# Kernel optimization log

Measured on AMD Instinct MI355X. Metric: run time of the kernel, lower is better.

The kernel has to match this reference:

```python
import jax, jax.numpy as jnp
import numpy as np


def setup_inputs() -> dict:
    key = jax.random.key(0)
    k1, k2 = jax.random.split(key)
    B, H, W, C = 32, 32, 32, 256
    N_EMBED = 1024
    z = jax.random.normal(k1, (B, H, W, C), dtype=jnp.float32)
    emb_weights = jax.random.normal(k2, (N_EMBED, C), dtype=jnp.float32)
    return {"z": z, "emb_weights": emb_weights}


def reference(z, emb_weights):
    # z: (B,H,W,C) -> flatten to (N, C)
    B = z.shape[0]
    C = z.shape[-1]
    z_flat = z.reshape(-1, C)  # (N, C)
    # Squared euclidean distance via ||z||^2 + ||e||^2 - 2 z.e^T
    distance = (
        jnp.sum(z_flat ** 2, axis=1, keepdims=True)          # (N, 1)
        + jnp.sum(emb_weights ** 2, axis=1)                   # (n_embed,)
        - 2.0 * jnp.dot(z_flat, emb_weights.T)                # (N, n_embed)
    )
    min_encoding_indices = jnp.argmin(distance, axis=1)       # (N,)
    z_q = emb_weights[min_encoding_indices].reshape(z.shape)  # (B,H,W,C)
    min_encoding_indices = min_encoding_indices.reshape(B, -1)
    return z_q, min_encoding_indices
```

## Files before the change

kernel.cpp:

```cpp
#include <hip/hip_runtime.h>

#define C_DIM 256
#define NCODE 1024
#define MARGIN1 0.35f
#define MARGIN2 0.02f

typedef __bf16 bf16x8 __attribute__((ext_vector_type(8)));
typedef float f32x4 __attribute__((ext_vector_type(4)));

#define WS_ENORM  0
#define WS_META   4096
#define WS_RLIST  8192
#define WS_RLIST2 139264
#define WS_BP     270336
#define WS_PB     1318912
#define WS_PBI    1843200
#define WS_PB2    2105344
#define WS_PBI2   3153920

#define BP_LO_OFF 262144

#define GLOAD_LDS16(g, s)                                                            \
  __builtin_amdgcn_global_load_lds(                                                  \
      (const __attribute__((address_space(1))) unsigned int*)(g),                    \
      (__attribute__((address_space(3))) unsigned int*)(s), 16, 0, 0)

__device__ __forceinline__ unsigned short bf16rne(float x) {
    unsigned u = __float_as_uint(x);
    return (unsigned short)((u + 0x7FFFu + ((u >> 16) & 1u)) >> 16);
}
__device__ __forceinline__ void bf16split(float x, unsigned short& h, unsigned short& l) {
    unsigned u  = __float_as_uint(x);
    unsigned rh = (u + 0x7FFFu + ((u >> 16) & 1u)) & 0xFFFF0000u;
    float    lf = x - __uint_as_float(rh);
    h = (unsigned short)(rh >> 16);
    l = bf16rne(lf);
}

__global__ __launch_bounds__(256) void prep_kernel(const float* __restrict__ emb,
                                                   unsigned short* __restrict__ bp,
                                                   float* __restrict__ enorm,
                                                   unsigned* __restrict__ meta) {
    int tid = blockIdx.x * 256 + threadIdx.x;
    if (tid < 2) meta[tid] = 0u;
    int j   = tid >> 5;
    int u   = tid & 31;
    int kc  = u >> 2, lg = u & 3;
    const float* src = emb + (size_t)j * C_DIM + kc * 32 + lg * 8;
    float4 v0 = *reinterpret_cast<const float4*>(src);
    float4 v1 = *reinterpret_cast<const float4*>(src + 4);
    float vs[8] = {v0.x, v0.y, v0.z, v0.w, v1.x, v1.y, v1.z, v1.w};
    unsigned short h[8], l[8];
    float s = 0.f;
    #pragma unroll
    for (int k = 0; k < 8; ++k) {
        bf16split(vs[k], h[k], l[k]);
        s = fmaf(vs[k], vs[k], s);
    }
    #pragma unroll
    for (int off = 1; off < 32; off <<= 1) s += __shfl_xor(s, off, 64);
    if (u == 0) enorm[j] = s;

    int chunk = j >> 5, nf = (j >> 4) & 1, lr = j & 15;
    int lane  = lg * 16 + lr;
    size_t base = (size_t)chunk * 8192 + (size_t)(nf * 8 + kc) * 512 + lane * 8;
    uint4 hp, lp;
    hp.x = (unsigned)h[0] | ((unsigned)h[1] << 16);
    hp.y = (unsigned)h[2] | ((unsigned)h[3] << 16);
    hp.z = (unsigned)h[4] | ((unsigned)h[5] << 16);
    hp.w = (unsigned)h[6] | ((unsigned)h[7] << 16);
    lp.x = (unsigned)l[0] | ((unsigned)l[1] << 16);
    lp.y = (unsigned)l[2] | ((unsigned)l[3] << 16);
    lp.z = (unsigned)l[4] | ((unsigned)l[5] << 16);
    lp.w = (unsigned)l[6] | ((unsigned)l[7] << 16);
    *reinterpret_cast<uint4*>(bp + base)             = hp;
    *reinterpret_cast<uint4*>(bp + BP_LO_OFF + base) = lp;
}

__global__ __launch_bounds__(256, 2) void vq_stage1_kernel(
    const float* __restrict__ z, const unsigned short* __restrict__ bp,
    const float* __restrict__ enorm, float2* __restrict__ pb,
    unsigned* __restrict__ pbi) {
    __shared__ unsigned short Bds[4][8192];
    __shared__ float en_s[512];

    const int t = threadIdx.x;
    const int w = t >> 6, lane = t & 63;
    const int lr = lane & 15, lg = lane >> 4;
    const int nh = blockIdx.x & 1;
    const long r0 = (long)(blockIdx.x >> 1) * 128 + w * 32;
    const unsigned short* bsrc = bp + (size_t)(nh * 16) * 8192 + lane * 8;

    en_s[t]       = enorm[nh * 512 + t];
    en_s[t + 256] = enorm[nh * 512 + 256 + t];

    bf16x8 ah[2][8];
    #pragma unroll
    for (int m = 0; m < 2; ++m) {
        const float* zr = z + (r0 + m * 16 + lr) * C_DIM + lg * 8;
        #pragma unroll
        for (int kc = 0; kc < 8; ++kc) {
            float4 v0 = *reinterpret_cast<const float4*>(zr + kc * 32);
            float4 v1 = *reinterpret_cast<const float4*>(zr + kc * 32 + 4);
            float vs[8] = {v0.x, v0.y, v0.z, v0.w, v1.x, v1.y, v1.z, v1.w};
            unsigned hp[4];
            #pragma unroll
            for (int p = 0; p < 4; ++p)
                hp[p] = (unsigned)bf16rne(vs[2 * p]) |
                        ((unsigned)bf16rne(vs[2 * p + 1]) << 16);
            ah[m][kc] = __builtin_bit_cast(bf16x8, *reinterpret_cast<uint4*>(hp));
        }
    }
    __syncthreads();

#define STG1(c) {                                                       \
    unsigned short* db = &Bds[(c) & 3][0];                              \
    const unsigned short* gs = bsrc + (size_t)(c) * 8192;               \
    _Pragma("unroll") for (int rd = 0; rd < 4; ++rd) {                  \
        int s_ = rd * 4 + w;                                            \
        GLOAD_LDS16(gs + s_ * 512, db + s_ * 512); } }

    STG1(0); STG1(1); STG1(2);

    float b1[2][4], b2[2][4]; unsigned i1[2][4];
    #pragma unroll
    for (int m = 0; m < 2; ++m)
        #pragma unroll
        for (int r = 0; r < 4; ++r) { b1[m][r] = 3.4e38f; b2[m][r] = 3.4e38f; i1[m][r] = 0; }

    #pragma unroll 1
    for (int c = 0; c < 16; ++c) {
        if (c <= 13)      { asm volatile("s_waitcnt vmcnt(8)" ::: "memory"); }
        else if (c == 14) { asm volatile("s_waitcnt vmcnt(4)" ::: "memory"); }
        else              { asm volatile("s_waitcnt vmcnt(0)" ::: "memory"); }
        __builtin_amdgcn_s_barrier();
        if (c < 13) STG1(c + 3);

        f32x4 a00 = {0.f,0.f,0.f,0.f}, a01 = {0.f,0.f,0.f,0.f};
        f32x4 a10 = {0.f,0.f,0.f,0.f}, a11 = {0.f,0.f,0.f,0.f};
        const unsigned short* bb = &Bds[c & 3][lane * 8];
        __builtin_amdgcn_s_setprio(1);
        #pragma unroll
        for (int kc = 0; kc < 8; ++kc) {
            bf16x8 bh0 = *reinterpret_cast<const bf16x8*>(bb + kc * 512);
            bf16x8 bh1 = *reinterpret_cast<const bf16x8*>(bb + (8 + kc) * 512);
            a00 = __builtin_amdgcn_mfma_f32_16x16x32_bf16(ah[0][kc], bh0, a00, 0, 0, 0);
            a10 = __builtin_amdgcn_mfma_f32_16x16x32_bf16(ah[1][kc], bh0, a10, 0, 0, 0);
            a01 = __builtin_amdgcn_mfma_f32_16x16x32_bf16(ah[0][kc], bh1, a01, 0, 0, 0);
            a11 = __builtin_amdgcn_mfma_f32_16x16x32_bf16(ah[1][kc], bh1, a11, 0, 0, 0);
        }
        __builtin_amdgcn_s_setprio(0);

        #pragma unroll
        for (int nf = 0; nf < 2; ++nf) {
            const int cl = c * 32 + nf * 16 + lr;
            const float en = en_s[cl];
            const unsigned code = (unsigned)(nh * 512 + cl);
            #pragma unroll
            for (int r = 0; r < 4; ++r) {
                float d0 = fmaf(-2.f, (nf ? a01[r] : a00[r]), en);
                if (d0 < b1[0][r]) { b2[0][r] = b1[0][r]; b1[0][r] = d0; i1[0][r] = code; }
                else if (d0 < b2[0][r]) { b2[0][r] = d0; }
                float d1 = fmaf(-2.f, (nf ? a11[r] : a10[r]), en);
                if (d1 < b1[1][r]) { b2[1][r] = b1[1][r]; b1[1][r] = d1; i1[1][r] = code; }
                else if (d1 < b2[1][r]) { b2[1][r] = d1; }
            }
        }
    }
#undef STG1

    #pragma unroll
    for (int m = 0; m < 2; ++m)
        #pragma unroll
        for (int r = 0; r < 4; ++r) {
            float v1 = b1[m][r], v2 = b2[m][r]; unsigned j1 = i1[m][r];
            #pragma unroll
            for (int off = 8; off; off >>= 1) {
                float    ov1 = __shfl_xor(v1, off, 64);
                float    ov2 = __shfl_xor(v2, off, 64);
                unsigned oj1 = (unsigned)__shfl_xor((int)j1, off, 64);
                if (ov1 < v1 || (ov1 == v1 && oj1 < j1)) {
                    v2 = fminf(v1, ov2); v1 = ov1; j1 = oj1;
                } else {
                    v2 = fminf(v2, ov1);
                }
            }
            if (lr == 0) {
                long row = r0 + m * 16 + lg * 4 + r;
                pb [row * 2 + nh] = make_float2(v1, v2);
                pbi[row * 2 + nh] = j1;
            }
        }
}

__global__ __launch_bounds__(256) void finalize_gather_kernel(
    const float* __restrict__ emb, const float2* __restrict__ pb,
    const unsigned* __restrict__ pbi, float* __restrict__ zq,
    float* __restrict__ idx_out, unsigned* __restrict__ meta,
    unsigned* __restrict__ rlist) {
    const long row = (long)blockIdx.x * 4 + (threadIdx.x >> 6);
    const int lane = threadIdx.x & 63;
    float2   p0 = pb [row * 2 + 0], p1 = pb [row * 2 + 1];
    unsigned j0 = pbi[row * 2 + 0], j1 = pbi[row * 2 + 1];
    float B1, B2; unsigned I1;
    if (p1.x < p0.x) { B1 = p1.x; I1 = j1; B2 = fminf(p0.x, p1.y); }
    else             { B1 = p0.x; I1 = j0; B2 = fminf(p0.y, p1.x); }
    if (lane == 0) {
        idx_out[row] = (float)I1;
        if (B2 - B1 <= MARGIN1) rlist[atomicAdd(meta, 1u)] = (unsigned)row;
    }
    float4 v = reinterpret_cast<const float4*>(emb)[(size_t)I1 * 64 + lane];
    reinterpret_cast<float4*>(zq)[row * 64 + lane] = v;
}

__global__ __launch_bounds__(256) void vq_stage2_kernel(
    const float* __restrict__ z, const unsigned short* __restrict__ bp,
    const float* __restrict__ enorm, const unsigned* __restrict__ meta,
    const unsigned* __restrict__ rlist, float2* __restrict__ pb2,
    unsigned* __restrict__ pbi2) {
    __shared__ float en_s[NCODE];
    const int t = threadIdx.x, w = t >> 6, lane = t & 63;
    const int lr = lane & 15, lg = lane >> 4;
    en_s[t] = enorm[t]; en_s[t + 256] = enorm[t + 256];
    en_s[t + 512] = enorm[t + 512]; en_s[t + 768] = enorm[t + 768];
    __syncthreads();
    const unsigned cnt = meta[0];
    const unsigned nitems = ((cnt + 15) >> 4) << 2;

    for (unsigned item = blockIdx.x * 4 + (unsigned)w; item < nitems;
         item += gridDim.x * 4) {
        const unsigned g = item >> 2, q = item & 3;
        const unsigned base = g * 16;
        unsigned slot = base + (unsigned)lr;
        unsigned row = rlist[slot < cnt ? slot : 0];

        bf16x8 ah[8], al[8];
        const float* zr = z + (size_t)row * C_DIM + lg * 8;
        #pragma unroll
        for (int kc = 0; kc < 8; ++kc) {
            float4 v0 = *reinterpret_cast<const float4*>(zr + kc * 32);
            float4 v1 = *reinterpret_cast<const float4*>(zr + kc * 32 + 4);
            float vs[8] = {v0.x, v0.y, v0.z, v0.w, v1.x, v1.y, v1.z, v1.w};
            unsigned short hv[8], lv[8];
            #pragma unroll
            for (int jj = 0; jj < 8; ++jj) bf16split(vs[jj], hv[jj], lv[jj]);
            unsigned hp[4] = {
                (unsigned)hv[0] | ((unsigned)hv[1] << 16), (unsigned)hv[2] | ((unsigned)hv[3] << 16),
                (unsigned)hv[4] | ((unsigned)hv[5] << 16), (unsigned)hv[6] | ((unsigned)hv[7] << 16)};
            unsigned lp[4] = {
                (unsigned)lv[0] | ((unsigned)lv[1] << 16), (unsigned)lv[2] | ((unsigned)lv[3] << 16),
                (unsigned)lv[4] | ((unsigned)lv[5] << 16), (unsigned)lv[6] | ((unsigned)lv[7] << 16)};
            ah[kc] = __builtin_bit_cast(bf16x8, *reinterpret_cast<uint4*>(hp));
            al[kc] = __builtin_bit_cast(bf16x8, *reinterpret_cast<uint4*>(lp));
        }

        float b1[4], b2[4]; unsigned i1[4];
        #pragma unroll
        for (int r = 0; r < 4; ++r) { b1[r] = 3.4e38f; b2[r] = 3.4e38f; i1[r] = 0; }

        #pragma unroll 1
        for (int cc = 0; cc < 8; ++cc) {
            const int c = (int)q * 8 + cc;
            f32x4 hh0 = {0.f,0.f,0.f,0.f}, hh1 = {0.f,0.f,0.f,0.f};
            f32x4 hl0 = {0.f,0.f,0.f,0.f}, hl1 = {0.f,0.f,0.f,0.f};
            f32x4 lh0 = {0.f,0.f,0.f,0.f}, lh1 = {0.f,0.f,0.f,0.f};
            const unsigned short* cb = bp + (size_t)c * 8192 + lane * 8;
            #pragma unroll
            for (int kc = 0; kc < 8; ++kc) {
                bf16x8 bh0 = *reinterpret_cast<const bf16x8*>(cb + kc * 512);
                bf16x8 bh1 = *reinterpret_cast<const bf16x8*>(cb + (8 + kc) * 512);
                bf16x8 bl0 = *reinterpret_cast<const bf16x8*>(cb + BP_LO_OFF + kc * 512);
                bf16x8 bl1 = *reinterpret_cast<const bf16x8*>(cb + BP_LO_OFF + (8 + kc) * 512);
                hh0 = __builtin_amdgcn_mfma_f32_16x16x32_bf16(ah[kc], bh0, hh0, 0, 0, 0);
                hh1 = __builtin_amdgcn_mfma_f32_16x16x32_bf16(ah[kc], bh1, hh1, 0, 0, 0);
                lh0 = __builtin_amdgcn_mfma_f32_16x16x32_bf16(al[kc], bh0, lh0, 0, 0, 0);
                lh1 = __builtin_amdgcn_mfma_f32_16x16x32_bf16(al[kc], bh1, lh1, 0, 0, 0);
                hl0 = __builtin_amdgcn_mfma_f32_16x16x32_bf16(ah[kc], bl0, hl0, 0, 0, 0);
                hl1 = __builtin_amdgcn_mfma_f32_16x16x32_bf16(ah[kc], bl1, hl1, 0, 0, 0);
            }
            #pragma unroll
            for (int nf = 0; nf < 2; ++nf) {
                const unsigned code = (unsigned)(c * 32 + nf * 16 + lr);
                const float en = en_s[code];
                #pragma unroll
                for (int r = 0; r < 4; ++r) {
                    float s3 = nf ? (hh1[r] + hl1[r] + lh1[r]) : (hh0[r] + hl0[r] + lh0[r]);
                    float d = fmaf(-2.f, s3, en);
                    if (d < b1[r]) { b2[r] = b1[r]; b1[r] = d; i1[r] = code; }
                    else if (d < b2[r]) { b2[r] = d; }
                }
            }
        }

        #pragma unroll
        for (int r = 0; r < 4; ++r) {
            float v1 = b1[r], v2 = b2[r]; unsigned j1 = i1[r];
            #pragma unroll
            for (int off = 8; off; off >>= 1) {
                float    ov1 = __shfl_xor(v1, off, 64);
                float    ov2 = __shfl_xor(v2, off, 64);
                unsigned oj1 = (unsigned)__shfl_xor((int)j1, off, 64);
                if (ov1 < v1 || (ov1 == v1 && oj1 < j1)) {
                    v2 = fminf(v1, ov2); v1 = ov1; j1 = oj1;
                } else {
                    v2 = fminf(v2, ov1);
                }
            }
            if (lr == 0) {
                unsigned sl = base + (unsigned)(lg * 4 + r);
                if (sl < cnt) {
                    pb2 [sl * 4 + q] = make_float2(v1, v2);
                    pbi2[sl * 4 + q] = j1;
                }
            }
        }
    }
}

__global__ __launch_bounds__(256) void finalize2_kernel(
    const float* __restrict__ emb, const unsigned* __restrict__ meta,
    const unsigned* __restrict__ rlist, const float2* __restrict__ pb2,
    const unsigned* __restrict__ pbi2, float* __restrict__ zq,
    float* __restrict__ idx_out, unsigned* __restrict__ meta2,
    unsigned* __restrict__ rlist2) {
    const int w = threadIdx.x >> 6, lane = threadIdx.x & 63;
    const unsigned cnt = meta[0];
    for (unsigned slot = blockIdx.x * 4 + (unsigned)w; slot < cnt;
         slot += gridDim.x * 4) {
        unsigned row = rlist[slot];
        float B1 = 3.4e38f, B2 = 3.4e38f; unsigned I1 = 0;
        #pragma unroll
        for (int s = 0; s < 4; ++s) {
            float2   p = pb2 [slot * 4 + s];
            unsigned j = pbi2[slot * 4 + s];
            if (p.x < B1) { B2 = fminf(B1, p.y); B1 = p.x; I1 = j; }
            else          { B2 = fminf(B2, p.x); }
        }
        if (lane == 0) {
            idx_out[row] = (float)I1;
            if (B2 - B1 <= MARGIN2) rlist2[atomicAdd(meta2, 1u)] = row;
        }
        float4 v = reinterpret_cast<const float4*>(emb)[(size_t)I1 * 64 + lane];
        reinterpret_cast<float4*>(zq)[(size_t)row * 64 + lane] = v;
    }
}

__global__ __launch_bounds__(256) void rescue_kernel(
    const float* __restrict__ z, const float* __restrict__ emb,
    const float* __restrict__ enorm, const unsigned* __restrict__ meta2,
    const unsigned* __restrict__ rlist2, float* __restrict__ zq,
    float* __restrict__ idx_out) {
    __shared__ float zrow[C_DIM];
    __shared__ float rd[256];
    __shared__ unsigned rix[256];
    const unsigned cnt = meta2[0];
    for (unsigned li = blockIdx.x; li < cnt; li += gridDim.x) {
        unsigned row = rlist2[li];
        __syncthreads();
        if (threadIdx.x < 64) {
            float4 v = reinterpret_cast<const float4*>(z)[(size_t)row * 64 + threadIdx.x];
            reinterpret_cast<float4*>(zrow)[threadIdx.x] = v;
        }
        __syncthreads();
        const int c = threadIdx.x;
        float a0 = 0.f, a1 = 0.f, a2 = 0.f, a3 = 0.f;
        const float4* zp = reinterpret_cast<const float4*>(zrow);
        const float4* e0 = reinterpret_cast<const float4*>(emb + (size_t)(c)       * C_DIM);
        const float4* e1 = reinterpret_cast<const float4*>(emb + (size_t)(c + 256) * C_DIM);
        const float4* e2 = reinterpret_cast<const float4*>(emb + (size_t)(c + 512) * C_DIM);
        const float4* e3 = reinterpret_cast<const float4*>(emb + (size_t)(c + 768) * C_DIM);
        #pragma unroll 8
        for (int k = 0; k < 64; ++k) {
            float4 z4 = zp[k];
            float4 f0 = e0[k], f1 = e1[k], f2 = e2[k], f3 = e3[k];
            a0 = fmaf(z4.x, f0.x, a0); a0 = fmaf(z4.y, f0.y, a0);
            a0 = fmaf(z4.z, f0.z, a0); a0 = fmaf(z4.w, f0.w, a0);
            a1 = fmaf(z4.x, f1.x, a1); a1 = fmaf(z4.y, f1.y, a1);
            a1 = fmaf(z4.z, f1.z, a1); a1 = fmaf(z4.w, f1.w, a1);
            a2 = fmaf(z4.x, f2.x, a2); a2 = fmaf(z4.y, f2.y, a2);
            a2 = fmaf(z4.z, f2.z, a2); a2 = fmaf(z4.w, f2.w, a2);
            a3 = fmaf(z4.x, f3.x, a3); a3 = fmaf(z4.y, f3.y, a3);
            a3 = fmaf(z4.z, f3.z, a3); a3 = fmaf(z4.w, f3.w, a3);
        }
        float d0 = fmaf(-2.f, a0, enorm[c]);
        float d1 = fmaf(-2.f, a1, enorm[c + 256]);
        float d2 = fmaf(-2.f, a2, enorm[c + 512]);
        float d3 = fmaf(-2.f, a3, enorm[c + 768]);
        float bd = d0; unsigned bi = (unsigned)c;
        if (d1 < bd) { bd = d1; bi = (unsigned)(c + 256); }
        if (d2 < bd) { bd = d2; bi = (unsigned)(c + 512); }
        if (d3 < bd) { bd = d3; bi = (unsigned)(c + 768); }
        rd[threadIdx.x] = bd; rix[threadIdx.x] = bi;
        __syncthreads();
        for (int s = 128; s; s >>= 1) {
            if (threadIdx.x < (unsigned)s) {
                float od = rd[threadIdx.x + s]; unsigned oi = rix[threadIdx.x + s];
                if (od < rd[threadIdx.x] ||
                    (od == rd[threadIdx.x] && oi < rix[threadIdx.x])) {
                    rd[threadIdx.x] = od; rix[threadIdx.x] = oi;
                }
            }
            __syncthreads();
        }
        unsigned code = rix[0];
        if (threadIdx.x < 64) {
            float4 v = reinterpret_cast<const float4*>(emb)[(size_t)code * 64 + threadIdx.x];
            reinterpret_cast<float4*>(zq)[(size_t)row * 64 + threadIdx.x] = v;
        }
        if (threadIdx.x == 0) idx_out[row] = (float)code;
    }
}

extern "C" void kernel_launch(void* const* d_in, const int* in_sizes, int n_in,
                              void* d_out, int out_size, void* d_ws, size_t ws_size,
                              hipStream_t stream) {
    const float* z   = (const float*)d_in[0];
    const float* emb = (const float*)d_in[1];
    const int n = in_sizes[0] / C_DIM;

    float* zq      = (float*)d_out;
    float* idx_out = zq + (size_t)n * C_DIM;

    char* ws = (char*)d_ws;
    float*          enorm  = (float*)(ws + WS_ENORM);
    unsigned*       meta   = (unsigned*)(ws + WS_META);
    unsigned*       rlist  = (unsigned*)(ws + WS_RLIST);
    unsigned*       rlist2 = (unsigned*)(ws + WS_RLIST2);
    unsigned short* bp     = (unsigned short*)(ws + WS_BP);
    float2*         pb     = (float2*)(ws + WS_PB);
    unsigned*       pbi    = (unsigned*)(ws + WS_PBI);
    float2*         pb2    = (float2*)(ws + WS_PB2);
    unsigned*       pbi2   = (unsigned*)(ws + WS_PBI2);

    prep_kernel<<<128, 256, 0, stream>>>(emb, bp, enorm, meta);
    vq_stage1_kernel<<<(n / 128) * 2, 256, 0, stream>>>(z, bp, enorm, pb, pbi);
    finalize_gather_kernel<<<n / 4, 256, 0, stream>>>(emb, pb, pbi, zq, idx_out,
                                                      meta, rlist);
    vq_stage2_kernel<<<512, 256, 0, stream>>>(z, bp, enorm, meta, rlist, pb2, pbi2);
    finalize2_kernel<<<512, 256, 0, stream>>>(emb, meta, rlist, pb2, pbi2,
                                              zq, idx_out, meta + 1, rlist2);
    rescue_kernel<<<256, 256, 0, stream>>>(z, emb, enorm, meta + 1, rlist2,
                                           zq, idx_out);
}
```

Before: 134.1 us.

## Fuse stage-2 finalize into stage-2 kernel and shrink stage-1 LDS ring

Stage 1 now uses a three-slot LDS ring instead of four, prefetching two chunks ahead, so it can allow three blocks per CU. Stage 2 gives each block one 16-row group, with the four waves covering codebook quarters. The waves reduce through shared memory, then write indices, the rescue list and gathered z_q rows directly, which removes the finalize2 kernel and its pb2/pbi2 workspace round trip. finalize_gather becomes a grid-stride loop over 2048 blocks. The cost is a shallower prefetch pipeline and extra block barriers in stage 2.

```diff
diff --git a/kernel.cpp b/kernel.cpp
--- a/kernel.cpp
+++ b/kernel.cpp
@@ -15,8 +15,6 @@
 #define WS_BP     270336
 #define WS_PB     1318912
 #define WS_PBI    1843200
-#define WS_PB2    2105344
-#define WS_PBI2   3153920
 
 #define BP_LO_OFF 262144
 
@@ -77,11 +75,11 @@
     *reinterpret_cast<uint4*>(bp + BP_LO_OFF + base) = lp;
 }
 
-__global__ __launch_bounds__(256, 2) void vq_stage1_kernel(
+__global__ __launch_bounds__(256, 3) void vq_stage1_kernel(
     const float* __restrict__ z, const unsigned short* __restrict__ bp,
     const float* __restrict__ enorm, float2* __restrict__ pb,
     unsigned* __restrict__ pbi) {
-    __shared__ unsigned short Bds[4][8192];
+    __shared__ unsigned short Bds[3][8192];
     __shared__ float en_s[512];
 
     const int t = threadIdx.x;
@@ -113,14 +111,14 @@
     }
     __syncthreads();
 
-#define STG1(c) {                                                       \
-    unsigned short* db = &Bds[(c) & 3][0];                              \
+#define STG1(c, sl) {                                                   \
+    unsigned short* db = &Bds[sl][0];                                   \
     const unsigned short* gs = bsrc + (size_t)(c) * 8192;               \
     _Pragma("unroll") for (int rd = 0; rd < 4; ++rd) {                  \
         int s_ = rd * 4 + w;                                            \
         GLOAD_LDS16(gs + s_ * 512, db + s_ * 512); } }
 
-    STG1(0); STG1(1); STG1(2);
+    STG1(0, 0); STG1(1, 1);
 
     float b1[2][4], b2[2][4]; unsigned i1[2][4];
     #pragma unroll
@@ -128,17 +126,17 @@
         #pragma unroll
         for (int r = 0; r < 4; ++r) { b1[m][r] = 3.4e38f; b2[m][r] = 3.4e38f; i1[m][r] = 0; }
 
+    int rs = 0, ws = 2;
     #pragma unroll 1
     for (int c = 0; c < 16; ++c) {
-        if (c <= 13)      { asm volatile("s_waitcnt vmcnt(8)" ::: "memory"); }
-        else if (c == 14) { asm volatile("s_waitcnt vmcnt(4)" ::: "memory"); }
-        else              { asm volatile("s_waitcnt vmcnt(0)" ::: "memory"); }
+        if (c <= 14) { asm volatile("s_waitcnt vmcnt(4)" ::: "memory"); }
+        else         { asm volatile("s_waitcnt vmcnt(0)" ::: "memory"); }
         __builtin_amdgcn_s_barrier();
-        if (c < 13) STG1(c + 3);
+        if (c < 14) STG1(c + 2, ws);
 
         f32x4 a00 = {0.f,0.f,0.f,0.f}, a01 = {0.f,0.f,0.f,0.f};
         f32x4 a10 = {0.f,0.f,0.f,0.f}, a11 = {0.f,0.f,0.f,0.f};
-        const unsigned short* bb = &Bds[c & 3][lane * 8];
+        const unsigned short* bb = &Bds[rs][lane * 8];
         __builtin_amdgcn_s_setprio(1);
         #pragma unroll
         for (int kc = 0; kc < 8; ++kc) {
@@ -166,6 +164,8 @@
                 else if (d1 < b2[1][r]) { b2[1][r] = d1; }
             }
         }
+        rs = rs + 1; if (rs == 3) rs = 0;
+        ws = ws + 1; if (ws == 3) ws = 0;
     }
 #undef STG1
 
@@ -197,39 +197,43 @@
     const float* __restrict__ emb, const float2* __restrict__ pb,
     const unsigned* __restrict__ pbi, float* __restrict__ zq,
     float* __restrict__ idx_out, unsigned* __restrict__ meta,
-    unsigned* __restrict__ rlist) {
-    const long row = (long)blockIdx.x * 4 + (threadIdx.x >> 6);
+    unsigned* __restrict__ rlist, int n4) {
     const int lane = threadIdx.x & 63;
-    float2   p0 = pb [row * 2 + 0], p1 = pb [row * 2 + 1];
-    unsigned j0 = pbi[row * 2 + 0], j1 = pbi[row * 2 + 1];
-    float B1, B2; unsigned I1;
-    if (p1.x < p0.x) { B1 = p1.x; I1 = j1; B2 = fminf(p0.x, p1.y); }
-    else             { B1 = p0.x; I1 = j0; B2 = fminf(p0.y, p1.x); }
-    if (lane == 0) {
-        idx_out[row] = (float)I1;
-        if (B2 - B1 <= MARGIN1) rlist[atomicAdd(meta, 1u)] = (unsigned)row;
-    }
-    float4 v = reinterpret_cast<const float4*>(emb)[(size_t)I1 * 64 + lane];
-    reinterpret_cast<float4*>(zq)[row * 64 + lane] = v;
+    for (long r4 = blockIdx.x; r4 < n4; r4 += gridDim.x) {
+        const long row = r4 * 4 + (threadIdx.x >> 6);
+        float2   p0 = pb [row * 2 + 0], p1 = pb [row * 2 + 1];
+        unsigned j0 = pbi[row * 2 + 0], j1 = pbi[row * 2 + 1];
+        float B1, B2; unsigned I1;
+        if (p1.x < p0.x) { B1 = p1.x; I1 = j1; B2 = fminf(p0.x, p1.y); }
+        else             { B1 = p0.x; I1 = j0; B2 = fminf(p0.y, p1.x); }
+        if (lane == 0) {
+            idx_out[row] = (float)I1;
+            if (B2 - B1 <= MARGIN1) rlist[atomicAdd(meta, 1u)] = (unsigned)row;
+        }
+        float4 v = reinterpret_cast<const float4*>(emb)[(size_t)I1 * 64 + lane];
+        reinterpret_cast<float4*>(zq)[row * 64 + lane] = v;
+    }
 }
 
 __global__ __launch_bounds__(256) void vq_stage2_kernel(
     const float* __restrict__ z, const unsigned short* __restrict__ bp,
-    const float* __restrict__ enorm, const unsigned* __restrict__ meta,
-    const unsigned* __restrict__ rlist, float2* __restrict__ pb2,
-    unsigned* __restrict__ pbi2) {
+    const float* __restrict__ enorm, const float* __restrict__ emb,
+    const unsigned* __restrict__ meta, const unsigned* __restrict__ rlist,
+    float* __restrict__ zq, float* __restrict__ idx_out,
+    unsigned* __restrict__ meta2, unsigned* __restrict__ rlist2) {
     __shared__ float en_s[NCODE];
-    const int t = threadIdx.x, w = t >> 6, lane = t & 63;
+    __shared__ float m1s[16][4], m2s[16][4];
+    __shared__ unsigned mis[16][4];
+    __shared__ unsigned codes_s[16];
+    const int t = threadIdx.x, q = t >> 6, lane = t & 63;
     const int lr = lane & 15, lg = lane >> 4;
     en_s[t] = enorm[t]; en_s[t + 256] = enorm[t + 256];
     en_s[t + 512] = enorm[t + 512]; en_s[t + 768] = enorm[t + 768];
     __syncthreads();
     const unsigned cnt = meta[0];
-    const unsigned nitems = ((cnt + 15) >> 4) << 2;
-
-    for (unsigned item = blockIdx.x * 4 + (unsigned)w; item < nitems;
-         item += gridDim.x * 4) {
-        const unsigned g = item >> 2, q = item & 3;
+    const unsigned ngroups = (cnt + 15) >> 4;
+
+    for (unsigned g = blockIdx.x; g < ngroups; g += gridDim.x) {
         const unsigned base = g * 16;
         unsigned slot = base + (unsigned)lr;
         unsigned row = rlist[slot < cnt ? slot : 0];
@@ -260,7 +264,7 @@
 
         #pragma unroll 1
         for (int cc = 0; cc < 8; ++cc) {
-            const int c = (int)q * 8 + cc;
+            const int c = q * 8 + cc;
             f32x4 hh0 = {0.f,0.f,0.f,0.f}, hh1 = {0.f,0.f,0.f,0.f};
             f32x4 hl0 = {0.f,0.f,0.f,0.f}, hl1 = {0.f,0.f,0.f,0.f};
             f32x4 lh0 = {0.f,0.f,0.f,0.f}, lh1 = {0.f,0.f,0.f,0.f};
@@ -307,41 +311,40 @@
                 }
             }
             if (lr == 0) {
-                unsigned sl = base + (unsigned)(lg * 4 + r);
-                if (sl < cnt) {
-                    pb2 [sl * 4 + q] = make_float2(v1, v2);
-                    pbi2[sl * 4 + q] = j1;
-                }
-            }
-        }
-    }
-}
-
-__global__ __launch_bounds__(256) void finalize2_kernel(
-    const float* __restrict__ emb, const unsigned* __restrict__ meta,
-    const unsigned* __restrict__ rlist, const float2* __restrict__ pb2,
-    const unsigned* __restrict__ pbi2, float* __restrict__ zq,
-    float* __restrict__ idx_out, unsigned* __restrict__ meta2,
-    unsigned* __restrict__ rlist2) {
-    const int w = threadIdx.x >> 6, lane = threadIdx.x & 63;
-    const unsigned cnt = meta[0];
-    for (unsigned slot = blockIdx.x * 4 + (unsigned)w; slot < cnt;
-         slot += gridDim.x * 4) {
-        unsigned row = rlist[slot];
-        float B1 = 3.4e38f, B2 = 3.4e38f; unsigned I1 = 0;
-        #pragma unroll
-        for (int s = 0; s < 4; ++s) {
-            float2   p = pb2 [slot * 4 + s];
-            unsigned j = pbi2[slot * 4 + s];
-            if (p.x < B1) { B2 = fminf(B1, p.y); B1 = p.x; I1 = j; }
-            else          { B2 = fminf(B2, p.x); }
-        }
-        if (lane == 0) {
-            idx_out[row] = (float)I1;
-            if (B2 - B1 <= MARGIN2) rlist2[atomicAdd(meta2, 1u)] = row;
-        }
-        float4 v = reinterpret_cast<const float4*>(emb)[(size_t)I1 * 64 + lane];
-        reinterpret_cast<float4*>(zq)[(size_t)row * 64 + lane] = v;
+                int rg = lg * 4 + r;
+                m1s[rg][q] = v1; m2s[rg][q] = v2; mis[rg][q] = j1;
+            }
+        }
+        __syncthreads();
+        if (t < 16) {
+            float B1 = 3.4e38f, B2 = 3.4e38f; unsigned I1 = 0;
+            #pragma unroll
+            for (int s = 0; s < 4; ++s) {
+                float v1 = m1s[t][s], v2 = m2s[t][s]; unsigned j = mis[t][s];
+                if (v1 < B1) { B2 = fminf(B1, v2); B1 = v1; I1 = j; }
+                else         { B2 = fminf(B2, v1); }
+            }
+            unsigned sl = base + (unsigned)t;
+            codes_s[t] = I1;
+            if (sl < cnt) {
+                unsigned rrow = rlist[sl];
+                idx_out[rrow] = (float)I1;
+                if (B2 - B1 <= MARGIN2) rlist2[atomicAdd(meta2, 1u)] = rrow;
+            }
+        }
+        __syncthreads();
+        {
+            int rr = t >> 4, seg = t & 15;
+            unsigned sl = base + (unsigned)rr;
+            if (sl < cnt) {
+                unsigned rrow = rlist[sl];
+                unsigned code = codes_s[rr];
+                const float4* ep = reinterpret_cast<const float4*>(emb) + (size_t)code * 64 + seg * 4;
+                float4*       op = reinterpret_cast<float4*>(zq) + (size_t)rrow * 64 + seg * 4;
+                op[0] = ep[0]; op[1] = ep[1]; op[2] = ep[2]; op[3] = ep[3];
+            }
+        }
+        __syncthreads();
     }
 }
 
@@ -429,15 +432,12 @@
     unsigned short* bp     = (unsigned short*)(ws + WS_BP);
     float2*         pb     = (float2*)(ws + WS_PB);
     unsigned*       pbi    = (unsigned*)(ws + WS_PBI);
-    float2*         pb2    = (float2*)(ws + WS_PB2);
-    unsigned*       pbi2   = (unsigned*)(ws + WS_PBI2);
 
     prep_kernel<<<128, 256, 0, stream>>>(emb, bp, enorm, meta);
     vq_stage1_kernel<<<(n / 128) * 2, 256, 0, stream>>>(z, bp, enorm, pb, pbi);
-    finalize_gather_kernel<<<n / 4, 256, 0, stream>>>(emb, pb, pbi, zq, idx_out,
-                                                      meta, rlist);
-    vq_stage2_kernel<<<512, 256, 0, stream>>>(z, bp, enorm, meta, rlist, pb2, pbi2);
-    finalize2_kernel<<<512, 256, 0, stream>>>(emb, meta, rlist, pb2, pbi2,
+    finalize_gather_kernel<<<2048, 256, 0, stream>>>(emb, pb, pbi, zq, idx_out,
+                                                     meta, rlist, n / 4);
+    vq_stage2_kernel<<<256, 256, 0, stream>>>(z, bp, enorm, emb, meta, rlist,
                                               zq, idx_out, meta + 1, rlist2);
     rescue_kernel<<<256, 256, 0, stream>>>(z, emb, enorm, meta + 1, rlist2,
                                            zq, idx_out);
```

Result: no change. 134.0 us (median of 2 runs) (-0.1%).
